# Kernel optimization log

Hardware: AMD Instinct MI355X
Metric: run time of the kernel (lower is better)

The kernel has to match this reference:

```python
import jax, jax.numpy as jnp
import numpy as np

CONT_FIELD = 13
CATE_FIELD = 26
VOCAB = 100000
EMB_DIM = 40
ATTN_DIM = 8
BATCH = 4096


def setup_inputs() -> dict:
    key = jax.random.key(0)
    ks = jax.random.split(key, 8)
    conts = jax.random.uniform(ks[0], (BATCH, CONT_FIELD), dtype=jnp.float32)
    cates = jax.random.randint(ks[1], (BATCH, CATE_FIELD), 0, VOCAB, dtype=jnp.int64)
    combs = jax.random.normal(ks[2], (BATCH, 1), dtype=jnp.float32)
    a = np.square(3.0 / (CATE_FIELD * EMB_DIM))
    emb_table = jax.random.uniform(ks[3], (VOCAB, EMB_DIM), minval=-a, maxval=a, dtype=jnp.float32)
    attn_W = jax.random.normal(ks[4], (ATTN_DIM, EMB_DIM), dtype=jnp.float32) * 0.1
    attn_b = jnp.zeros((ATTN_DIM,), dtype=jnp.float32)
    proj_W = jax.random.normal(ks[5], (1, ATTN_DIM), dtype=jnp.float32) * 0.3
    fc_W = jax.random.normal(ks[6], (1, EMB_DIM), dtype=jnp.float32) * 0.1
    fc_b = jnp.zeros((1,), dtype=jnp.float32)
    return {"conts": conts, "cates": cates, "combs": combs, "emb_table": emb_table,
            "attn_W": attn_W, "attn_b": attn_b, "proj_W": proj_W, "fc_W": fc_W, "fc_b": fc_b}


def reference(conts, cates, combs, emb_table, attn_W, attn_b, proj_W, fc_W, fc_b):
    # continuous fields use fixed embedding rows 0..CONT_FIELD-1 scaled by value
    cont_emb = emb_table[jnp.arange(CONT_FIELD)][None, :, :] * conts[:, :, None]  # (B, 13, D)
    cate_emb = emb_table[cates]                                                   # (B, 26, D)
    x = jnp.concatenate([cont_emb, cate_emb], axis=1)                             # (B, 39, D)
    row, col = jnp.triu_indices(CONT_FIELD + CATE_FIELD, k=1)                     # 741 pairs
    ewp = x[:, row, :] * x[:, col, :]                                             # (B, 741, D)
    h = jax.nn.relu(jnp.einsum('bpd,ad->bpa', ewp, attn_W) + attn_b)              # (B, 741, 8)
    logits = jnp.einsum('bpa,oa->bpo', h, proj_W)                                 # (B, 741, 1)
    attn = jax.nn.softmax(logits, axis=1)                                         # softmax over pairs
    pooled = jnp.sum(attn * ewp, axis=1)                                          # (B, D)
    out = jax.nn.sigmoid(pooled @ fc_W.T + fc_b)                                  # (B, 1)
    return out
```

## Files before the change

kernel.cpp:

```cpp
#include <hip/hip_runtime.h>
#include <math.h>

#define NF 39
#define CONT_F 13
#define CATE_F 26
#define EMB_D 40
#define VOCAB 100000
#define NCH 9
#define ROW_B 80
#define CH_B  3120

typedef __attribute__((ext_vector_type(8))) short short8;
typedef __attribute__((ext_vector_type(4))) float f32x4;

__device__ __forceinline__ unsigned pack_bf16x2_trunc(float a, float b) {
    return (__float_as_uint(b) & 0xFFFF0000u) | (__float_as_uint(a) >> 16);
}

__global__ __launch_bounds__(192, 3)
void afm_mfma_kernel(const float* __restrict__ conts,
                     const int*   __restrict__ cates,
                     const float* __restrict__ emb,
                     const float* __restrict__ attn_W,
                     const float* __restrict__ attn_b,
                     const float* __restrict__ proj_W,
                     const float* __restrict__ fc_W,
                     const float* __restrict__ fc_b,
                     float* __restrict__ out)
{
    __shared__ __attribute__((aligned(16))) unsigned short Xb[NF * EMB_D];
    __shared__ __attribute__((aligned(16))) unsigned short Aall[NCH * NF * EMB_D];
    __shared__ __attribute__((aligned(16))) float zero16[4];
    __shared__ float reds[3], redg[3];

    const int tid = threadIdx.x;
    const int row = blockIdx.x;

    if (tid < 4) zero16[tid] = 0.f;

    {
        const float4* emb4 = (const float4*)emb;
        unsigned* XbW = (unsigned*)Xb;
        unsigned* AW  = (unsigned*)Aall;
        for (int t = tid; t < NF * 10; t += 192) {
            const int f = t / 10, q = t % 10;
            float4 v;
            if (f < CONT_F) {
                v = emb4[f * 10 + q];
                const float cs = conts[row * CONT_F + f];
                v.x *= cs; v.y *= cs; v.z *= cs; v.w *= cs;
            } else {
                unsigned u = (unsigned)cates[row * CATE_F + (f - CONT_F)];
                if (u >= (unsigned)VOCAB) u = 0;
                v = emb4[u * 10 + q];
            }
            const int wofs = f * 20 + q * 2;
            *(uint2*)&XbW[wofs] = make_uint2(pack_bf16x2_trunc(v.x, v.y),
                                             pack_bf16x2_trunc(v.z, v.w));
            #pragma unroll
            for (int c = 0; c < NCH; ++c) {
                const float4 wv = (c < 8) ? ((const float4*)attn_W)[c * 10 + q]
                                          : ((const float4*)fc_W)[q];
                *(uint2*)&AW[c * 780 + wofs] =
                    make_uint2(pack_bf16x2_trunc(v.x * wv.x, v.y * wv.y),
                               pack_bf16x2_trunc(v.z * wv.z, v.w * wv.w));
            }
        }
    }
    __syncthreads();

    const int wid  = tid >> 6;
    const int lane = tid & 63;
    const int l15  = lane & 15;
    const int quad = lane >> 4;

    int rA = wid * 16 + l15; if (rA > NF - 1) rA = NF - 1;

    const char* XbP = (const char*)Xb;
    const char* AP  = (const char*)Aall;
    const char* ZP  = (const char*)zero16;

    short8 b0[3], b1[3];
    #pragma unroll
    for (int nt = 0; nt < 3; ++nt) {
        if (nt >= wid) {
            int rB = nt * 16 + l15; if (rB > NF - 1) rB = NF - 1;
            b0[nt] = *(const short8*)(XbP + rB * ROW_B + quad * 16);
            b1[nt] = *(const short8*)((quad == 0) ? (XbP + rB * ROW_B + 64) : ZP);
        }
    }

    float pj[8], bb[8];
    #pragma unroll
    for (int a = 0; a < 8; ++a) { pj[a] = proj_W[a]; bb[a] = attn_b[a]; }

    float lacc[3][4] = {{0}};
    float gv[3][4];

    #pragma unroll
    for (int c = 0; c < NCH; ++c) {
        const char* aRow = AP + c * CH_B + rA * ROW_B;
        const short8 a0 = *(const short8*)(aRow + quad * 16);
        const short8 a1 = *(const short8*)((quad == 0) ? (aRow + 64) : ZP);
        f32x4 z[3];
        #pragma unroll
        for (int nt = 0; nt < 3; ++nt) {
            if (nt >= wid) {
                f32x4 t = {0.f, 0.f, 0.f, 0.f};
                t = __builtin_amdgcn_mfma_f32_16x16x32_bf16(a0, b0[nt], t, 0, 0, 0);
                t = __builtin_amdgcn_mfma_f32_16x16x32_bf16(a1, b1[nt], t, 0, 0, 0);
                z[nt] = t;
            }
        }
        #pragma unroll
        for (int nt = 0; nt < 3; ++nt) {
            if (nt >= wid) {
                #pragma unroll
                for (int r = 0; r < 4; ++r) {
                    if (c < 8)
                        lacc[nt][r] = fmaf(pj[c], fmaxf(z[nt][r] + bb[c], 0.f),
                                           lacc[nt][r]);
                    else
                        gv[nt][r] = z[nt][r];
                }
            }
        }
    }

    float s = 0.f, gs = 0.f;
    #pragma unroll
    for (int nt = 0; nt < 3; ++nt) {
        if (nt >= wid) {
            #pragma unroll
            for (int r = 0; r < 4; ++r) {
                const int i = wid * 16 + quad * 4 + r;
                const int j = nt * 16 + l15;
                if (i < j && j < NF) {
                    const float e = __expf(lacc[nt][r]);
                    s += e;
                    gs = fmaf(e, gv[nt][r], gs);
                }
            }
        }
    }
    #pragma unroll
    for (int off = 32; off; off >>= 1) {
        s  += __shfl_xor(s, off);
        gs += __shfl_xor(gs, off);
    }
    if (lane == 0) { reds[wid] = s; redg[wid] = gs; }
    __syncthreads();

    if (tid == 0) {
        const float S = reds[0] + reds[1] + reds[2];
        const float G = redg[0] + redg[1] + redg[2];
        const float zf = G / S + fc_b[0];
        out[row] = 1.f / (1.f + __expf(-zf));
    }
}

extern "C" void kernel_launch(void* const* d_in, const int* in_sizes, int n_in,
                              void* d_out, int out_size, void* d_ws, size_t ws_size,
                              hipStream_t stream) {
    const float* conts  = (const float*)d_in[0];
    const int*   cates  = (const int*)  d_in[1];
    const float* emb    = (const float*)d_in[3];
    const float* attn_W = (const float*)d_in[4];
    const float* attn_b = (const float*)d_in[5];
    const float* proj_W = (const float*)d_in[6];
    const float* fc_W   = (const float*)d_in[7];
    const float* fc_b   = (const float*)d_in[8];
    float* out = (float*)d_out;

    const int batch = in_sizes[0] / CONT_F;
    afm_mfma_kernel<<<batch, 192, 0, stream>>>(
        conts, cates, emb, attn_W, attn_b, proj_W, fc_W, fc_b, out);
}
```

Measured before the change: 104.5 us.

## Make kernel persistent with software-pipelined embedding gather across rows

Switches from one block per batch row to a grid of at most 1024 blocks that loop over rows. The next row's index loads and embedding gathers are issued before the current row's MFMA and softmax work, so gather latency overlaps with compute. Weights are staged once in LDS instead of being reloaded from global per element, and bf16 packing now uses a single perm instruction. This adds register pressure and an extra barrier per row, and leaves each CU with fewer resident blocks to hide latency.

```diff
diff --git a/kernel.cpp b/kernel.cpp
--- a/kernel.cpp
+++ b/kernel.cpp
@@ -9,15 +9,17 @@
 #define NCH 9
 #define ROW_B 80
 #define CH_B  3120
+#define BLK_T 192
+#define GRID_MAX 1024
 
 typedef __attribute__((ext_vector_type(8))) short short8;
 typedef __attribute__((ext_vector_type(4))) float f32x4;
 
-__device__ __forceinline__ unsigned pack_bf16x2_trunc(float a, float b) {
-    return (__float_as_uint(b) & 0xFFFF0000u) | (__float_as_uint(a) >> 16);
+__device__ __forceinline__ unsigned pk2(float a, float b) {
+    return __builtin_amdgcn_perm(__float_as_uint(b), __float_as_uint(a), 0x07060302u);
 }
 
-__global__ __launch_bounds__(192, 3)
+__global__ __launch_bounds__(BLK_T, 3)
 void afm_mfma_kernel(const float* __restrict__ conts,
                      const int*   __restrict__ cates,
                      const float* __restrict__ emb,
@@ -26,136 +28,182 @@
                      const float* __restrict__ proj_W,
                      const float* __restrict__ fc_W,
                      const float* __restrict__ fc_b,
-                     float* __restrict__ out)
+                     float* __restrict__ out,
+                     int batch)
 {
     __shared__ __attribute__((aligned(16))) unsigned short Xb[NF * EMB_D];
     __shared__ __attribute__((aligned(16))) unsigned short Aall[NCH * NF * EMB_D];
+    __shared__ __attribute__((aligned(16))) float Wlds[NCH * 10 * 4];
     __shared__ __attribute__((aligned(16))) float zero16[4];
     __shared__ float reds[3], redg[3];
 
     const int tid = threadIdx.x;
-    const int row = blockIdx.x;
+    const float4* emb4 = (const float4*)emb;
 
     if (tid < 4) zero16[tid] = 0.f;
-
-    {
-        const float4* emb4 = (const float4*)emb;
+    if (tid < NCH * 10) {
+        const int c = tid / 10, q = tid % 10;
+        ((float4*)Wlds)[tid] = (c < 8) ? ((const float4*)attn_W)[c * 10 + q]
+                                       : ((const float4*)fc_W)[q];
+    }
+
+    int f_[3], q_[3], wofs[3];
+    #pragma unroll
+    for (int k = 0; k < 3; ++k) {
+        const int t = tid + k * BLK_T;
+        const int f = t / 10;
+        f_[k] = f; q_[k] = t - f * 10;
+        wofs[k] = f * 20 + q_[k] * 2;
+    }
+    const bool act2  = (tid < 6);
+    const bool cont0 = (tid < 130);
+
+    const int stride = gridDim.x;
+    int r = blockIdx.x;
+
+    float  csI0;  int uI[3];
+    float4 vaG[3]; float csG0;
+
+    auto idx_load = [&](int rowi) {
+        if (cont0) { csI0 = conts[rowi * CONT_F + f_[0]]; }
+        else {
+            unsigned u = (unsigned)cates[rowi * CATE_F + (f_[0] - CONT_F)];
+            uI[0] = (u >= (unsigned)VOCAB) ? 0 : (int)u;
+        }
+        {
+            unsigned u = (unsigned)cates[rowi * CATE_F + (f_[1] - CONT_F)];
+            uI[1] = (u >= (unsigned)VOCAB) ? 0 : (int)u;
+        }
+        if (act2) {
+            unsigned u = (unsigned)cates[rowi * CATE_F + (f_[2] - CONT_F)];
+            uI[2] = (u >= (unsigned)VOCAB) ? 0 : (int)u;
+        }
+    };
+    auto gather = [&]() {
+        const int er0 = cont0 ? f_[0] : uI[0];
+        vaG[0] = emb4[er0 * 10 + q_[0]];
+        csG0   = cont0 ? csI0 : 1.f;
+        vaG[1] = emb4[uI[1] * 10 + q_[1]];
+        if (act2) vaG[2] = emb4[uI[2] * 10 + q_[2]];
+    };
+    auto pack_item = [&](float4 v, float cs, int wofsk, int qk) {
+        v.x *= cs; v.y *= cs; v.z *= cs; v.w *= cs;
         unsigned* XbW = (unsigned*)Xb;
         unsigned* AW  = (unsigned*)Aall;
-        for (int t = tid; t < NF * 10; t += 192) {
-            const int f = t / 10, q = t % 10;
-            float4 v;
-            if (f < CONT_F) {
-                v = emb4[f * 10 + q];
-                const float cs = conts[row * CONT_F + f];
-                v.x *= cs; v.y *= cs; v.z *= cs; v.w *= cs;
-            } else {
-                unsigned u = (unsigned)cates[row * CATE_F + (f - CONT_F)];
-                if (u >= (unsigned)VOCAB) u = 0;
-                v = emb4[u * 10 + q];
-            }
-            const int wofs = f * 20 + q * 2;
-            *(uint2*)&XbW[wofs] = make_uint2(pack_bf16x2_trunc(v.x, v.y),
-                                             pack_bf16x2_trunc(v.z, v.w));
-            #pragma unroll
-            for (int c = 0; c < NCH; ++c) {
-                const float4 wv = (c < 8) ? ((const float4*)attn_W)[c * 10 + q]
-                                          : ((const float4*)fc_W)[q];
-                *(uint2*)&AW[c * 780 + wofs] =
-                    make_uint2(pack_bf16x2_trunc(v.x * wv.x, v.y * wv.y),
-                               pack_bf16x2_trunc(v.z * wv.z, v.w * wv.w));
-            }
-        }
-    }
-    __syncthreads();
+        *(uint2*)&XbW[wofsk] = make_uint2(pk2(v.x, v.y), pk2(v.z, v.w));
+        #pragma unroll
+        for (int c = 0; c < NCH; ++c) {
+            const float4 wv = ((const float4*)Wlds)[c * 10 + qk];
+            *(uint2*)&AW[c * 780 + wofsk] =
+                make_uint2(pk2(v.x * wv.x, v.y * wv.y), pk2(v.z * wv.z, v.w * wv.w));
+        }
+    };
+    auto pack_write = [&]() {
+        pack_item(vaG[0], csG0, wofs[0], q_[0]);
+        pack_item(vaG[1], 1.f,  wofs[1], q_[1]);
+        if (act2) pack_item(vaG[2], 1.f, wofs[2], q_[2]);
+    };
 
     const int wid  = tid >> 6;
     const int lane = tid & 63;
     const int l15  = lane & 15;
     const int quad = lane >> 4;
-
     int rA = wid * 16 + l15; if (rA > NF - 1) rA = NF - 1;
 
     const char* XbP = (const char*)Xb;
     const char* AP  = (const char*)Aall;
     const char* ZP  = (const char*)zero16;
 
-    short8 b0[3], b1[3];
-    #pragma unroll
-    for (int nt = 0; nt < 3; ++nt) {
-        if (nt >= wid) {
-            int rB = nt * 16 + l15; if (rB > NF - 1) rB = NF - 1;
-            b0[nt] = *(const short8*)(XbP + rB * ROW_B + quad * 16);
-            b1[nt] = *(const short8*)((quad == 0) ? (XbP + rB * ROW_B + 64) : ZP);
-        }
-    }
-
     float pj[8], bb[8];
     #pragma unroll
     for (int a = 0; a < 8; ++a) { pj[a] = proj_W[a]; bb[a] = attn_b[a]; }
-
-    float lacc[3][4] = {{0}};
-    float gv[3][4];
-
-    #pragma unroll
-    for (int c = 0; c < NCH; ++c) {
-        const char* aRow = AP + c * CH_B + rA * ROW_B;
-        const short8 a0 = *(const short8*)(aRow + quad * 16);
-        const short8 a1 = *(const short8*)((quad == 0) ? (aRow + 64) : ZP);
-        f32x4 z[3];
+    const float fcb = fc_b[0];
+
+    idx_load(r);
+    gather();
+    { int rn = r + stride; idx_load(rn < batch ? rn : 0); }
+    __syncthreads();
+    pack_write();
+    __syncthreads();
+
+    for (;;) {
+        const int rn = r + stride;
+        const bool hn = (rn < batch);
+
+        if (hn) gather();
+        { int r2 = rn + stride; idx_load(r2 < batch ? r2 : 0); }
+
+        short8 b0[3], b1[3];
         #pragma unroll
         for (int nt = 0; nt < 3; ++nt) {
             if (nt >= wid) {
-                f32x4 t = {0.f, 0.f, 0.f, 0.f};
-                t = __builtin_amdgcn_mfma_f32_16x16x32_bf16(a0, b0[nt], t, 0, 0, 0);
-                t = __builtin_amdgcn_mfma_f32_16x16x32_bf16(a1, b1[nt], t, 0, 0, 0);
-                z[nt] = t;
+                int rB = nt * 16 + l15; if (rB > NF - 1) rB = NF - 1;
+                b0[nt] = *(const short8*)(XbP + rB * ROW_B + quad * 16);
+                b1[nt] = *(const short8*)((quad == 0) ? (XbP + rB * ROW_B + 64) : ZP);
             }
         }
+
+        float lacc[3][4] = {{0.f}};
+        float gv[3][4];
+        #pragma unroll
+        for (int c = 0; c < NCH; ++c) {
+            const char* aRow = AP + c * CH_B + rA * ROW_B;
+            const short8 a0 = *(const short8*)(aRow + quad * 16);
+            const short8 a1 = *(const short8*)((quad == 0) ? (aRow + 64) : ZP);
+            #pragma unroll
+            for (int nt = 0; nt < 3; ++nt) {
+                if (nt >= wid) {
+                    f32x4 t = {0.f, 0.f, 0.f, 0.f};
+                    t = __builtin_amdgcn_mfma_f32_16x16x32_bf16(a0, b0[nt], t, 0, 0, 0);
+                    t = __builtin_amdgcn_mfma_f32_16x16x32_bf16(a1, b1[nt], t, 0, 0, 0);
+                    #pragma unroll
+                    for (int rr = 0; rr < 4; ++rr) {
+                        if (c < 8)
+                            lacc[nt][rr] = fmaf(pj[c], fmaxf(t[rr] + bb[c], 0.f),
+                                                lacc[nt][rr]);
+                        else
+                            gv[nt][rr] = t[rr];
+                    }
+                }
+            }
+        }
+
+        float s = 0.f, gs = 0.f;
         #pragma unroll
         for (int nt = 0; nt < 3; ++nt) {
             if (nt >= wid) {
                 #pragma unroll
-                for (int r = 0; r < 4; ++r) {
-                    if (c < 8)
-                        lacc[nt][r] = fmaf(pj[c], fmaxf(z[nt][r] + bb[c], 0.f),
-                                           lacc[nt][r]);
-                    else
-                        gv[nt][r] = z[nt][r];
+                for (int rr = 0; rr < 4; ++rr) {
+                    const int i = wid * 16 + quad * 4 + rr;
+                    const int j = nt * 16 + l15;
+                    if (i < j && j < NF) {
+                        const float e = __expf(lacc[nt][rr]);
+                        s += e;
+                        gs = fmaf(e, gv[nt][rr], gs);
+                    }
                 }
             }
         }
-    }
-
-    float s = 0.f, gs = 0.f;
-    #pragma unroll
-    for (int nt = 0; nt < 3; ++nt) {
-        if (nt >= wid) {
-            #pragma unroll
-            for (int r = 0; r < 4; ++r) {
-                const int i = wid * 16 + quad * 4 + r;
-                const int j = nt * 16 + l15;
-                if (i < j && j < NF) {
-                    const float e = __expf(lacc[nt][r]);
-                    s += e;
-                    gs = fmaf(e, gv[nt][r], gs);
-                }
-            }
-        }
-    }
-    #pragma unroll
-    for (int off = 32; off; off >>= 1) {
-        s  += __shfl_xor(s, off);
-        gs += __shfl_xor(gs, off);
-    }
-    if (lane == 0) { reds[wid] = s; redg[wid] = gs; }
-    __syncthreads();
-
-    if (tid == 0) {
-        const float S = reds[0] + reds[1] + reds[2];
-        const float G = redg[0] + redg[1] + redg[2];
-        const float zf = G / S + fc_b[0];
-        out[row] = 1.f / (1.f + __expf(-zf));
+        #pragma unroll
+        for (int off = 32; off; off >>= 1) {
+            s  += __shfl_xor(s, off);
+            gs += __shfl_xor(gs, off);
+        }
+        if (lane == 0) { reds[wid] = s; redg[wid] = gs; }
+        __syncthreads();
+
+        if (tid == 0) {
+            const float S = reds[0] + reds[1] + reds[2];
+            const float G = redg[0] + redg[1] + redg[2];
+            const float zf = G / S + fcb;
+            out[r] = 1.f / (1.f + __expf(-zf));
+        }
+
+        if (hn) pack_write();
+        __syncthreads();
+
+        if (!hn) break;
+        r = rn;
     }
 }
 
@@ -173,6 +221,7 @@
     float* out = (float*)d_out;
 
     const int batch = in_sizes[0] / CONT_F;
-    afm_mfma_kernel<<<batch, 192, 0, stream>>>(
-        conts, cates, emb, attn_W, attn_b, proj_W, fc_W, fc_b, out);
+    int grid = batch < GRID_MAX ? batch : GRID_MAX;
+    afm_mfma_kernel<<<grid, BLK_T, 0, stream>>>(
+        conts, cates, emb, attn_W, attn_b, proj_W, fc_W, fc_b, out, batch);
 }
```

After: 101.6 us. 1.03x faster.

## Process one batch row per wavefront with register-resident MFMA fragments

Applied to the files above, without the earlier changes.

Changes the mapping from one 192-thread block per batch row to one wavefront per row, with four rows per 256-thread block. Each lane loads its embedding rows straight into registers and builds the bf16 MFMA operands there, which removes the per-row LDS staging, the block barriers and the cross-wave reduction. The attention bias is folded into the MFMA through an extra ones column. The cost is that each wave now computes all six upper-triangular tiles itself, which raises register pressure and duplicates the weight-scaled operand packing per lane.

```diff
diff --git a/kernel.cpp b/kernel.cpp
--- a/kernel.cpp
+++ b/kernel.cpp
@@ -7,18 +7,18 @@
 #define EMB_D 40
 #define VOCAB 100000
 #define NCH 9
-#define ROW_B 80
-#define CH_B  3120
 
 typedef __attribute__((ext_vector_type(8))) short short8;
 typedef __attribute__((ext_vector_type(4))) float f32x4;
 
-__device__ __forceinline__ unsigned pack_bf16x2_trunc(float a, float b) {
-    return (__float_as_uint(b) & 0xFFFF0000u) | (__float_as_uint(a) >> 16);
+union frag { short8 s; uint4 u; };
+
+__device__ __forceinline__ unsigned pk2(float a, float b) {
+    return __builtin_amdgcn_perm(__float_as_uint(b), __float_as_uint(a), 0x07060302u);
 }
 
-__global__ __launch_bounds__(192, 3)
-void afm_mfma_kernel(const float* __restrict__ conts,
+__global__ __launch_bounds__(256, 2)
+void afm_wave_kernel(const float* __restrict__ conts,
                      const int*   __restrict__ cates,
                      const float* __restrict__ emb,
                      const float* __restrict__ attn_W,
@@ -26,120 +26,129 @@
                      const float* __restrict__ proj_W,
                      const float* __restrict__ fc_W,
                      const float* __restrict__ fc_b,
-                     float* __restrict__ out)
+                     float* __restrict__ out,
+                     int batch)
 {
-    __shared__ __attribute__((aligned(16))) unsigned short Xb[NF * EMB_D];
-    __shared__ __attribute__((aligned(16))) unsigned short Aall[NCH * NF * EMB_D];
-    __shared__ __attribute__((aligned(16))) float zero16[4];
-    __shared__ float reds[3], redg[3];
+    __shared__ __attribute__((aligned(16))) float Wlds[NCH * EMB_D];
 
     const int tid = threadIdx.x;
-    const int row = blockIdx.x;
-
-    if (tid < 4) zero16[tid] = 0.f;
-
-    {
-        const float4* emb4 = (const float4*)emb;
-        unsigned* XbW = (unsigned*)Xb;
-        unsigned* AW  = (unsigned*)Aall;
-        for (int t = tid; t < NF * 10; t += 192) {
-            const int f = t / 10, q = t % 10;
-            float4 v;
-            if (f < CONT_F) {
-                v = emb4[f * 10 + q];
-                const float cs = conts[row * CONT_F + f];
-                v.x *= cs; v.y *= cs; v.z *= cs; v.w *= cs;
-            } else {
-                unsigned u = (unsigned)cates[row * CATE_F + (f - CONT_F)];
-                if (u >= (unsigned)VOCAB) u = 0;
-                v = emb4[u * 10 + q];
-            }
-            const int wofs = f * 20 + q * 2;
-            *(uint2*)&XbW[wofs] = make_uint2(pack_bf16x2_trunc(v.x, v.y),
-                                             pack_bf16x2_trunc(v.z, v.w));
-            #pragma unroll
-            for (int c = 0; c < NCH; ++c) {
-                const float4 wv = (c < 8) ? ((const float4*)attn_W)[c * 10 + q]
-                                          : ((const float4*)fc_W)[q];
-                *(uint2*)&AW[c * 780 + wofs] =
-                    make_uint2(pack_bf16x2_trunc(v.x * wv.x, v.y * wv.y),
-                               pack_bf16x2_trunc(v.z * wv.z, v.w * wv.w));
-            }
-        }
-    }
-    __syncthreads();
-
-    const int wid  = tid >> 6;
-    const int lane = tid & 63;
-    const int l15  = lane & 15;
-    const int quad = lane >> 4;
-
-    int rA = wid * 16 + l15; if (rA > NF - 1) rA = NF - 1;
-
-    const char* XbP = (const char*)Xb;
-    const char* AP  = (const char*)Aall;
-    const char* ZP  = (const char*)zero16;
-
-    short8 b0[3], b1[3];
-    #pragma unroll
-    for (int nt = 0; nt < 3; ++nt) {
-        if (nt >= wid) {
-            int rB = nt * 16 + l15; if (rB > NF - 1) rB = NF - 1;
-            b0[nt] = *(const short8*)(XbP + rB * ROW_B + quad * 16);
-            b1[nt] = *(const short8*)((quad == 0) ? (XbP + rB * ROW_B + 64) : ZP);
-        }
+    if (tid < NCH * 10) {
+        const int c = tid / 10, q = tid % 10;
+        ((float4*)Wlds)[tid] = (c < 8) ? ((const float4*)attn_W)[c * 10 + q]
+                                       : ((const float4*)fc_W)[q];
     }
 
     float pj[8], bb[8];
     #pragma unroll
     for (int a = 0; a < 8; ++a) { pj[a] = proj_W[a]; bb[a] = attn_b[a]; }
+    const float fcb = fc_b[0];
 
-    float lacc[3][4] = {{0}};
-    float gv[3][4];
+    __syncthreads();
+
+    const int wave = tid >> 6;
+    const int lane = tid & 63;
+    const int l15  = lane & 15;
+    const int quad = lane >> 4;
+    const int row  = blockIdx.x * 4 + wave;
+    if (row >= batch) return;
+
+    int erow[3];
+    float cs = 1.f;
+    const bool contl = (l15 < CONT_F);
+    if (contl) {
+        erow[0] = l15;
+        cs = conts[row * CONT_F + l15];
+    } else {
+        unsigned u = (unsigned)cates[row * CATE_F + (l15 - CONT_F)];
+        erow[0] = (u >= (unsigned)VOCAB) ? 0 : (int)u;
+    }
+    {
+        unsigned u = (unsigned)cates[row * CATE_F + (3 + l15)];
+        erow[1] = (u >= (unsigned)VOCAB) ? 0 : (int)u;
+    }
+    {
+        int f2 = 32 + l15; if (f2 > NF - 1) f2 = NF - 1;
+        unsigned u = (unsigned)cates[row * CATE_F + (f2 - CONT_F)];
+        erow[2] = (u >= (unsigned)VOCAB) ? 0 : (int)u;
+    }
+
+    float xf[3][8];
+    float xe[3][2];
+    #pragma unroll
+    for (int m = 0; m < 3; ++m) {
+        const char* rp = (const char*)emb + (size_t)erow[m] * 160;
+        const float4 h0 = *(const float4*)(rp + quad * 32);
+        const float4 h1 = *(const float4*)(rp + quad * 32 + 16);
+        const float2 t0 = *(const float2*)(rp + 128 + quad * 8);
+        xf[m][0] = h0.x; xf[m][1] = h0.y; xf[m][2] = h0.z; xf[m][3] = h0.w;
+        xf[m][4] = h1.x; xf[m][5] = h1.y; xf[m][6] = h1.z; xf[m][7] = h1.w;
+        xe[m][0] = t0.x; xe[m][1] = t0.y;
+    }
+    if (contl) {
+        #pragma unroll
+        for (int t = 0; t < 8; ++t) xf[0][t] *= cs;
+        xe[0][0] *= cs; xe[0][1] *= cs;
+    }
+
+    frag xb[3], xb2[3];
+    const unsigned onew = (quad == 0) ? pk2(1.0f, 0.0f) : 0u;
+    #pragma unroll
+    for (int m = 0; m < 3; ++m) {
+        xb[m].u = make_uint4(pk2(xf[m][0], xf[m][1]), pk2(xf[m][2], xf[m][3]),
+                             pk2(xf[m][4], xf[m][5]), pk2(xf[m][6], xf[m][7]));
+        xb2[m].u = make_uint4(pk2(xe[m][0], xe[m][1]), onew, 0u, 0u);
+    }
+
+    static const int TM[6] = {0, 0, 0, 1, 1, 2};
+    static const int TN[6] = {0, 1, 2, 1, 2, 2};
+    float lacc[6][4] = {{0.f}};
+    float gv[6][4];
 
     #pragma unroll
     for (int c = 0; c < NCH; ++c) {
-        const char* aRow = AP + c * CH_B + rA * ROW_B;
-        const short8 a0 = *(const short8*)(aRow + quad * 16);
-        const short8 a1 = *(const short8*)((quad == 0) ? (aRow + 64) : ZP);
-        f32x4 z[3];
+        const float* wrow = Wlds + c * EMB_D;
+        const float4 w0 = *(const float4*)(wrow + quad * 8);
+        const float4 w1 = *(const float4*)(wrow + quad * 8 + 4);
+        const float2 wt = *(const float2*)(wrow + 32 + quad * 2);
+        const unsigned bw = (quad == 0 && c < 8) ? pk2(bb[c], 0.0f) : 0u;
+
+        frag a0[3], a1[3];
         #pragma unroll
-        for (int nt = 0; nt < 3; ++nt) {
-            if (nt >= wid) {
-                f32x4 t = {0.f, 0.f, 0.f, 0.f};
-                t = __builtin_amdgcn_mfma_f32_16x16x32_bf16(a0, b0[nt], t, 0, 0, 0);
-                t = __builtin_amdgcn_mfma_f32_16x16x32_bf16(a1, b1[nt], t, 0, 0, 0);
-                z[nt] = t;
-            }
+        for (int m = 0; m < 3; ++m) {
+            a0[m].u = make_uint4(pk2(xf[m][0] * w0.x, xf[m][1] * w0.y),
+                                 pk2(xf[m][2] * w0.z, xf[m][3] * w0.w),
+                                 pk2(xf[m][4] * w1.x, xf[m][5] * w1.y),
+                                 pk2(xf[m][6] * w1.z, xf[m][7] * w1.w));
+            a1[m].u = make_uint4(pk2(xe[m][0] * wt.x, xe[m][1] * wt.y), bw, 0u, 0u);
         }
+
         #pragma unroll
-        for (int nt = 0; nt < 3; ++nt) {
-            if (nt >= wid) {
+        for (int tt = 0; tt < 6; ++tt) {
+            f32x4 t = {0.f, 0.f, 0.f, 0.f};
+            t = __builtin_amdgcn_mfma_f32_16x16x32_bf16(a0[TM[tt]].s, xb[TN[tt]].s, t, 0, 0, 0);
+            t = __builtin_amdgcn_mfma_f32_16x16x32_bf16(a1[TM[tt]].s, xb2[TN[tt]].s, t, 0, 0, 0);
+            if (c < 8) {
                 #pragma unroll
-                for (int r = 0; r < 4; ++r) {
-                    if (c < 8)
-                        lacc[nt][r] = fmaf(pj[c], fmaxf(z[nt][r] + bb[c], 0.f),
-                                           lacc[nt][r]);
-                    else
-                        gv[nt][r] = z[nt][r];
-                }
+                for (int rr = 0; rr < 4; ++rr)
+                    lacc[tt][rr] = fmaf(pj[c], fmaxf(t[rr], 0.f), lacc[tt][rr]);
+            } else {
+                #pragma unroll
+                for (int rr = 0; rr < 4; ++rr) gv[tt][rr] = t[rr];
             }
         }
     }
 
     float s = 0.f, gs = 0.f;
     #pragma unroll
-    for (int nt = 0; nt < 3; ++nt) {
-        if (nt >= wid) {
-            #pragma unroll
-            for (int r = 0; r < 4; ++r) {
-                const int i = wid * 16 + quad * 4 + r;
-                const int j = nt * 16 + l15;
-                if (i < j && j < NF) {
-                    const float e = __expf(lacc[nt][r]);
-                    s += e;
-                    gs = fmaf(e, gv[nt][r], gs);
-                }
+    for (int tt = 0; tt < 6; ++tt) {
+        #pragma unroll
+        for (int rr = 0; rr < 4; ++rr) {
+            const int i = TM[tt] * 16 + quad * 4 + rr;
+            const int j = TN[tt] * 16 + l15;
+            if (i < j && j < NF) {
+                const float e = __expf(lacc[tt][rr]);
+                s += e;
+                gs = fmaf(e, gv[tt][rr], gs);
             }
         }
     }
@@ -148,13 +157,8 @@
         s  += __shfl_xor(s, off);
         gs += __shfl_xor(gs, off);
     }
-    if (lane == 0) { reds[wid] = s; redg[wid] = gs; }
-    __syncthreads();
-
-    if (tid == 0) {
-        const float S = reds[0] + reds[1] + reds[2];
-        const float G = redg[0] + redg[1] + redg[2];
-        const float zf = G / S + fc_b[0];
+    if (lane == 0) {
+        const float zf = gs / s + fcb;
         out[row] = 1.f / (1.f + __expf(-zf));
     }
 }
@@ -173,6 +177,7 @@
     float* out = (float*)d_out;
 
     const int batch = in_sizes[0] / CONT_F;
-    afm_mfma_kernel<<<batch, 192, 0, stream>>>(
-        conts, cates, emb, attn_W, attn_b, proj_W, fc_W, fc_b, out);
+    const int grid = (batch + 3) / 4;
+    afm_wave_kernel<<<grid, 256, 0, stream>>>(
+        conts, cates, emb, attn_W, attn_b, proj_W, fc_W, fc_b, out, batch);
 }
```

After: 91.56 us. 1.14x faster.
